# Performance work log

Measured on AMD Instinct MI355X. Metric: run time of the kernel, lower is better.

The kernel has to match this reference:

```python
import jax, jax.numpy as jnp
import numpy as np

H = 56; W = 56; WS = 7; SS = 3; NH = 12; DIM = 384; B = 32
N = WS * WS                      # 49 tokens per window
NW = (H // WS) * (W // WS)       # 64 windows per image
HID = 4 * DIM
EPS = 1e-5


def _rel_index():
    coords = np.stack(np.meshgrid(np.arange(WS), np.arange(WS), indexing='ij'))  # [2,ws,ws]
    cf = coords.reshape(2, -1)
    rel = (cf[:, :, None] - cf[:, None, :]).transpose(1, 2, 0)  # [N,N,2]
    rel[..., 0] += WS - 1
    rel[..., 1] += WS - 1
    rel[..., 0] *= 2 * WS - 1
    return rel.sum(-1).astype(np.int32)  # [N,N] in [0,169)


def _attn_mask():
    img = np.zeros((H, W), np.float32)
    cnt = 0
    sl = (slice(0, -WS), slice(-WS, -SS), slice(-SS, None))
    for h in sl:
        for w in sl:
            img[h, w] = cnt
            cnt += 1
    mw = img.reshape(H // WS, WS, W // WS, WS).transpose(0, 2, 1, 3).reshape(-1, N)  # [nW,N]
    am = mw[:, None, :] - mw[:, :, None]  # [nW,N,N]
    return np.where(am != 0, np.float32(-100.0), np.float32(0.0)).astype(np.float32)


def _ln(x, g, b):
    m = jnp.mean(x, axis=-1, keepdims=True)
    v = jnp.mean(jnp.square(x - m), axis=-1, keepdims=True)
    return (x - m) * jax.lax.rsqrt(v + EPS) * g + b


def setup_inputs() -> dict:
    key = jax.random.key(0)
    ks = jax.random.split(key, 8)
    s = 0.02
    return {
        'x': jax.random.normal(ks[0], (B, H * W, DIM), jnp.float32),
        'qkv_w': jax.random.normal(ks[1], (3 * DIM, DIM), jnp.float32) * s,
        'qkv_b': jnp.zeros((3 * DIM,), jnp.float32),
        'proj_w': jax.random.normal(ks[2], (DIM, DIM), jnp.float32) * s,
        'proj_b': jnp.zeros((DIM,), jnp.float32),
        'rpb_table': jax.random.normal(ks[3], ((2 * WS - 1) ** 2, NH), jnp.float32) * s,
        'ln1_g': jnp.ones((DIM,), jnp.float32),
        'ln1_b': jnp.zeros((DIM,), jnp.float32),
        'fc1_w': jax.random.normal(ks[4], (HID, DIM), jnp.float32) * s,
        'fc1_b': jnp.zeros((HID,), jnp.float32),
        'fc2_w': jax.random.normal(ks[5], (DIM, HID), jnp.float32) * s,
        'fc2_b': jnp.zeros((DIM,), jnp.float32),
        'ln2_g': jnp.ones((DIM,), jnp.float32),
        'ln2_b': jnp.zeros((DIM,), jnp.float32),
        'attn_mask': jnp.asarray(_attn_mask()),
        'rel_idx': jnp.asarray(_rel_index()),
    }


def reference(x, qkv_w, qkv_b, proj_w, proj_b, rpb_table, ln1_g, ln1_b,
              fc1_w, fc1_b, fc2_w, fc2_b, ln2_g, ln2_b, attn_mask, rel_idx):
    Bb, L, C = x.shape
    hd = C // NH
    scale = hd ** -0.5
    shortcut = x
    # cyclic shift
    xs = jnp.roll(x.reshape(Bb, H, W, C), (-SS, -SS), axis=(1, 2))
    # window partition -> [Bb*nW, N, C]
    xw = xs.reshape(Bb, H // WS, WS, W // WS, WS, C).transpose(0, 1, 3, 2, 4, 5).reshape(-1, N, C)
    # qkv
    qkv = (xw @ qkv_w.T + qkv_b).reshape(-1, N, 3, NH, hd).transpose(2, 0, 3, 1, 4)
    q, k, v = qkv[0] * scale, qkv[1], qkv[2]          # [Bb*nW, NH, N, hd]
    attn = jnp.einsum('whnd,whmd->whnm', q, k)        # [Bb*nW, NH, N, N]
    bias = rpb_table[rel_idx.reshape(-1)].reshape(N, N, NH).transpose(2, 0, 1)
    attn = attn + bias[None]
    # shifted-window mask
    attn = attn.reshape(Bb, NW, NH, N, N) + attn_mask[None, :, None]
    attn = jax.nn.softmax(attn.reshape(-1, NH, N, N), axis=-1)
    out = jnp.einsum('whnm,whmd->whnd', attn, v).transpose(0, 2, 1, 3).reshape(-1, N, C)
    out = out @ proj_w.T + proj_b
    # window reverse + roll back
    xs = out.reshape(Bb, H // WS, W // WS, WS, WS, C).transpose(0, 1, 3, 2, 4, 5).reshape(Bb, H, W, C)
    xs = jnp.roll(xs, (SS, SS), axis=(1, 2)).reshape(Bb, L, C)
    # post-norm residuals (as in source: shortcut + norm(attn_out); x += norm(ffn(x)))
    x1 = shortcut + _ln(xs, ln1_g, ln1_b)
    y = jax.nn.gelu(x1 @ fc1_w.T + fc1_b, approximate=False) @ fc2_w.T + fc2_b
    return x1 + _ln(y, ln2_g, ln2_b)
```

## Files before the change

kernel.cpp:

```cpp
#include <hip/hip_runtime.h>
#include <hip/hip_bf16.h>
#include <math.h>

typedef __hip_bfloat16 bf16;
typedef __bf16 bf16x8 __attribute__((ext_vector_type(8)));
typedef float f32x4 __attribute__((ext_vector_type(4)));

#define HH 56
#define WW 56
#define WSZ 7
#define SSH 3
#define NHEAD 12
#define CDIM 384
#define BBATCH 32
#define NTOK 49
#define NWIN 64
#define HIDD 1536
#define HD 32
#define NWTOT (BBATCH*NWIN)
#define MROWS (NWTOT*NTOK)
#define MHALF (MROWS/2)
#define LTOT (HH*WW)
#define EPSLN 1e-5f
#define QSCALE 0.17677669529663687f
#define NEGBIG -1e30f

enum { M_QK = 0, M_V = 1, M_FC1 = 2 };

__device__ __forceinline__ void gload16(const void* g, void* l) {
    __builtin_amdgcn_global_load_lds(
        (const __attribute__((address_space(1))) void*)g,
        (__attribute__((address_space(3))) void*)l, 16, 0, 0);
}

__device__ __forceinline__ unsigned short bfbits(float v) {
    bf16 b = __float2bfloat16(v);
    return *reinterpret_cast<unsigned short*>(&b);
}

__device__ __forceinline__ float fast_gelu(float v) {
    return v / (1.0f + __expf(-1.59576912f * v * fmaf(0.044715f, v * v, 1.0f)));
}

__device__ __forceinline__ int xcd_swz(int orig, int nwg) {
    const int q = nwg >> 3, r = nwg & 7;
    const int xcd = orig & 7, loc = orig >> 3;
    return (xcd < r ? xcd * (q + 1) : r * (q + 1) + (xcd - r) * q) + loc;
}

__global__ __launch_bounds__(256) void cvt_k(const float* __restrict__ src,
                                             bf16* __restrict__ dst, int n) {
    int i = blockIdx.x * 256 + threadIdx.x;
    if (i < n) dst[i] = __float2bfloat16(src[i]);
}

__global__ __launch_bounds__(256)
void tbl_k(const float* __restrict__ rpb, const int* __restrict__ relidx,
           const float* __restrict__ amask, float* __restrict__ tbl) {
    int idx = blockIdx.x * 256 + threadIdx.x;
    int m = idx & 63, n = (idx >> 6) & 63;
    int h = (idx >> 12) % NHEAD, wi = idx / (64 * 64 * NHEAD);
    float v;
    if (m >= NTOK) v = NEGBIG;
    else if (n >= NTOK) v = 0.f;
    else v = rpb[relidx[n * NTOK + m] * NHEAD + h] + amask[((long)wi * NTOK + n) * NTOK + m];
    tbl[idx] = v;
}

__global__ __launch_bounds__(256) void gather_k(const float* __restrict__ x,
                                                bf16* __restrict__ xw, int rbase) {
    int idx = blockIdx.x * 256 + threadIdx.x;
    int rr_l = idx / 96, c4 = (idx % 96) * 4;
    int rr = rbase + rr_l;
    int w = rr / 49, ti = rr % 49;
    int b = w >> 6, wi = w & 63;
    int hy = (wi >> 3) * 7 + ti / 7;
    int hx = (wi & 7) * 7 + ti % 7;
    int sh = hy + SSH; if (sh >= HH) sh -= HH;
    int sw = hx + SSH; if (sw >= WW) sw -= WW;
    float4 v = *(const float4*)&x[((long)b * LTOT + sh * WW + sw) * CDIM + c4];
    ushort4 u = { bfbits(v.x), bfbits(v.y), bfbits(v.z), bfbits(v.w) };
    *(ushort4*)&xw[(long)rr_l * CDIM + c4] = u;
}

template<int MODE, int KDIM, int NTN>
__global__ __launch_bounds__(256, 4)
void mgemm_k(const bf16* __restrict__ A, const bf16* __restrict__ Wt,
             const float* __restrict__ bias, void* __restrict__ Outp)
{
    constexpr bool SWAP = (MODE != M_V);
    __shared__ bf16 As[2][128 * 32];
    __shared__ bf16 Bs[2][128 * 32];
    const int tid = threadIdx.x;
    const int wid = tid >> 6, lane = tid & 63;

    const int gid = xcd_swz(blockIdx.x, gridDim.x);
    const int m0 = (gid / NTN) * 128;
    const int n0 = (gid % NTN) * 128;

    const int strow = lane >> 2, stseg = lane & 3;
    const int swseg = stseg ^ ((strow >> 1) & 3);
    const bf16* Ag = A + (long)(m0 + wid * 32 + strow) * KDIM + swseg * 8;
    const bf16* Wg = Wt + (long)(n0 + wid * 32 + strow) * KDIM + swseg * 8;

    const int wr = (wid >> 1) * 64, wc = (wid & 1) * 64;
    const int l15 = lane & 15, g4 = lane >> 4;
    const int sa = g4 ^ ((l15 >> 1) & 3);

    f32x4 acc[4][4] = {};

    auto STAGE = [&](int b, int t) {
#pragma unroll
        for (int i = 0; i < 2; ++i)
            gload16(Ag + (long)(i * 16) * KDIM + t * 32, &As[b][(wid * 32 + i * 16) * 32]);
#pragma unroll
        for (int i = 0; i < 2; ++i)
            gload16(Wg + (long)(i * 16) * KDIM + t * 32, &Bs[b][(wid * 32 + i * 16) * 32]);
    };

    const int nt = KDIM / 32;
    STAGE(0, 0);
    STAGE(1, 1);
    asm volatile("s_waitcnt vmcnt(4)" ::: "memory");
    __builtin_amdgcn_s_barrier();

    int buf = 0;
    for (int t = 0; t < nt; ++t) {
        bf16x8 af[4], bfr[4];
#pragma unroll
        for (int i = 0; i < 4; ++i) {
            af[i]  = *(const bf16x8*)&As[buf][(wr + i * 16 + l15) * 32 + sa * 8];
            bfr[i] = *(const bf16x8*)&Bs[buf][(wc + i * 16 + l15) * 32 + sa * 8];
        }
        __builtin_amdgcn_sched_barrier(0);
        asm volatile("s_waitcnt lgkmcnt(0)" ::: "memory");
        __builtin_amdgcn_sched_barrier(0);
        __builtin_amdgcn_s_barrier();
        if (t + 2 < nt) STAGE(buf, t + 2);
#pragma unroll
        for (int mi = 0; mi < 4; ++mi)
#pragma unroll
            for (int ni = 0; ni < 4; ++ni) {
                if (SWAP)
                    acc[ni][mi] = __builtin_amdgcn_mfma_f32_16x16x32_bf16(
                        bfr[ni], af[mi], acc[ni][mi], 0, 0, 0);
                else
                    acc[mi][ni] = __builtin_amdgcn_mfma_f32_16x16x32_bf16(
                        af[mi], bfr[ni], acc[mi][ni], 0, 0, 0);
            }
        if (t + 2 < nt) { asm volatile("s_waitcnt vmcnt(4)" ::: "memory"); }
        else            { asm volatile("s_waitcnt vmcnt(0)" ::: "memory"); }
        __builtin_amdgcn_s_barrier();
        buf ^= 1;
    }

    if (MODE == M_V) {
#pragma unroll
        for (int mi = 0; mi < 4; ++mi) {
            const int mb = m0 + wr + mi * 16 + g4 * 4;
            const int wv_ = mb / 49, ti0 = mb - wv_ * 49;
#pragma unroll
            for (int ni = 0; ni < 4; ++ni) {
                const int n = n0 + wc + ni * 16 + l15;
                const int h = n >> 5, d = n & 31;
                const float bn = bias[n];
                float v4[4];
#pragma unroll
                for (int j = 0; j < 4; ++j) v4[j] = acc[mi][ni][j] + bn;
                if (ti0 <= 45) {
                    ushort4 u = { bfbits(v4[0]), bfbits(v4[1]), bfbits(v4[2]), bfbits(v4[3]) };
                    *(ushort4*)&((bf16*)Outp)[(((long)wv_ * NHEAD + h) * HD + d) * 64 + ti0] = u;
                } else {
#pragma unroll
                    for (int j = 0; j < 4; ++j) {
                        const int m = mb + j;
                        const int w2 = m / 49, ti = m - w2 * 49;
                        ((bf16*)Outp)[(((long)w2 * NHEAD + h) * HD + d) * 64 + ti]
                            = __float2bfloat16(v4[j]);
                    }
                }
            }
        }
    } else {
        long rowbase[4];
        int wq_[4], ti_[4];
#pragma unroll
        for (int mi = 0; mi < 4; ++mi) {
            const int m = m0 + wr + mi * 16 + l15;
            if (MODE == M_QK) { wq_[mi] = m / 49; ti_[mi] = m - wq_[mi] * 49; }
            else              { rowbase[mi] = (long)m * HIDD; }
        }
#pragma unroll
        for (int ni = 0; ni < 4; ++ni) {
            const int nb = n0 + wc + ni * 16 + g4 * 4;
            const float4 bn = *(const float4*)&bias[nb];
            const float bb[4] = { bn.x, bn.y, bn.z, bn.w };
#pragma unroll
            for (int mi = 0; mi < 4; ++mi) {
                float v4[4];
#pragma unroll
                for (int j = 0; j < 4; ++j) v4[j] = acc[ni][mi][j] + bb[j];
                if (MODE == M_FC1) {
#pragma unroll
                    for (int j = 0; j < 4; ++j) v4[j] = fast_gelu(v4[j]);
                } else if (MODE == M_QK) {
                    if (nb < CDIM) {
#pragma unroll
                        for (int j = 0; j < 4; ++j) v4[j] *= QSCALE;
                    }
                }
                ushort4 u = { bfbits(v4[0]), bfbits(v4[1]), bfbits(v4[2]), bfbits(v4[3]) };
                if (MODE == M_QK) {
                    const int which = nb >= CDIM;
                    const int hb = (nb - which * CDIM) >> 5, d0 = nb & 31;
                    *(ushort4*)&((bf16*)Outp)[
                        ((((long)wq_[mi] * 2 + which) * NHEAD + hb) * NTOK + ti_[mi]) * HD + d0] = u;
                } else {
                    *(ushort4*)&((bf16*)Outp)[rowbase[mi] + nb] = u;
                }
            }
        }
    }
}

template<int KDIM, bool SCATTER>
__global__ __launch_bounds__(512, 2)
void gemm_ln_k(const bf16* __restrict__ A, const bf16* __restrict__ Wt,
               const float* __restrict__ bias, const bf16* __restrict__ resid,
               const float* __restrict__ lng, const float* __restrict__ lnb,
               float* __restrict__ outf, bf16* __restrict__ outb, int mbase)
{
    __shared__ bf16 As[2][128 * 32];
    __shared__ bf16 Bs[2][384 * 32];
    __shared__ float lnp[1024];
    const int tid = threadIdx.x;
    const int wid = tid >> 6, lane = tid & 63;

    const int m0 = xcd_swz(blockIdx.x, gridDim.x) * 128;

    const int strow = tid >> 2, stseg = tid & 3;
    const int sws = stseg ^ ((strow >> 1) & 3);
    const bf16* Ag = A + (long)(m0 + strow) * KDIM + sws * 8;
    const bf16* Wg = Wt + (long)strow * KDIM + sws * 8;

    const int wm = wid >> 2, wn = wid & 3;
    const int wr = wm * 64, wc = wn * 96;
    const int l15 = lane & 15, g4 = lane >> 4;
    const int sa = g4 ^ ((l15 >> 1) & 3);

    f32x4 acc[6][4] = {};

    auto STAGE = [&](int b, int t) {
        gload16(Ag + t * 32, &As[b][strow * 32 + stseg * 8]);
#pragma unroll
        for (int p = 0; p < 3; ++p)
            gload16(Wg + (long)(p * 128) * KDIM + t * 32,
                    &Bs[b][(p * 128 + strow) * 32 + stseg * 8]);
    };

    const int nt = KDIM / 32;
    STAGE(0, 0);
    STAGE(1, 1);
    asm volatile("s_waitcnt vmcnt(4)" ::: "memory");
    __builtin_amdgcn_s_barrier();

    int buf = 0;
    for (int t = 0; t < nt; ++t) {
        bf16x8 af[4], bfr[6];
#pragma unroll
        for (int i = 0; i < 4; ++i)
            af[i] = *(const bf16x8*)&As[buf][(wr + i * 16 + l15) * 32 + sa * 8];
#pragma unroll
        for (int i = 0; i < 6; ++i)
            bfr[i] = *(const bf16x8*)&Bs[buf][(wc + i * 16 + l15) * 32 + sa * 8];
        __builtin_amdgcn_sched_barrier(0);
        asm volatile("s_waitcnt lgkmcnt(0)" ::: "memory");
        __builtin_amdgcn_sched_barrier(0);
        __builtin_amdgcn_s_barrier();
        if (t + 2 < nt) STAGE(buf, t + 2);
#pragma unroll
        for (int ni = 0; ni < 6; ++ni)
#pragma unroll
            for (int mi = 0; mi < 4; ++mi)
                acc[ni][mi] = __builtin_amdgcn_mfma_f32_16x16x32_bf16(
                    bfr[ni], af[mi], acc[ni][mi], 0, 0, 0);
        if (t + 2 < nt) { asm volatile("s_waitcnt vmcnt(4)" ::: "memory"); }
        else            { asm volatile("s_waitcnt vmcnt(0)" ::: "memory"); }
        __builtin_amdgcn_s_barrier();
        buf ^= 1;
    }

    float psum[4] = {}, psq[4] = {};
#pragma unroll
    for (int ni = 0; ni < 6; ++ni) {
        const int nb = wc + ni * 16 + g4 * 4;
        const float4 bn = *(const float4*)&bias[nb];
        const float bb[4] = { bn.x, bn.y, bn.z, bn.w };
#pragma unroll
        for (int mi = 0; mi < 4; ++mi)
#pragma unroll
            for (int j = 0; j < 4; ++j) {
                float v = acc[ni][mi][j] + bb[j];
                acc[ni][mi][j] = v;
                psum[mi] += v; psq[mi] += v * v;
            }
    }
#pragma unroll
    for (int mi = 0; mi < 4; ++mi) {
        psum[mi] += __shfl_xor(psum[mi], 16); psum[mi] += __shfl_xor(psum[mi], 32);
        psq[mi]  += __shfl_xor(psq[mi], 16);  psq[mi]  += __shfl_xor(psq[mi], 32);
    }
    if (g4 == 0) {
#pragma unroll
        for (int mi = 0; mi < 4; ++mi) {
            const int r = wr + mi * 16 + l15;
            lnp[wn * 128 + r] = psum[mi];
            lnp[512 + wn * 128 + r] = psq[mi];
        }
    }
    __syncthreads();

#pragma unroll
    for (int mi = 0; mi < 4; ++mi) {
        const int r = wr + mi * 16 + l15;
        const float s  = lnp[r] + lnp[128 + r] + lnp[256 + r] + lnp[384 + r];
        const float sq = lnp[512 + r] + lnp[640 + r] + lnp[768 + r] + lnp[896 + r];
        const float mean = s * (1.f / 384.f);
        const float rstd = rsqrtf(sq * (1.f / 384.f) - mean * mean + EPSLN);

        const long rl = m0 + r;
        long dst;
        if (SCATTER) {
            const int m = mbase + (int)rl;
            int w = m / 49, ti = m - w * 49;
            int b = w >> 6, wi = w & 63;
            int hy = (wi >> 3) * 7 + ti / 7;
            int hx = (wi & 7) * 7 + ti % 7;
            int dh = hy + SSH; if (dh >= HH) dh -= HH;
            int dw = hx + SSH; if (dw >= WW) dw -= WW;
            dst = (long)b * LTOT + dh * WW + dw - mbase;
        } else {
            dst = mbase + rl;
        }
#pragma unroll
        for (int ni = 0; ni < 6; ++ni) {
            const int c = wc + ni * 16 + g4 * 4;
            const float4 gv = *(const float4*)&lng[c];
            const float4 bv = *(const float4*)&lnb[c];
            ushort4 xv = *(const ushort4*)&resid[rl * CDIM + c];
            float x0 = __bfloat162float(*(bf16*)&xv.x);
            float x1 = __bfloat162float(*(bf16*)&xv.y);
            float x2 = __bfloat162float(*(bf16*)&xv.z);
            float x3 = __bfloat162float(*(bf16*)&xv.w);
            float r0 = x0 + (acc[ni][mi][0] - mean) * rstd * gv.x + bv.x;
            float r1 = x1 + (acc[ni][mi][1] - mean) * rstd * gv.y + bv.y;
            float r2 = x2 + (acc[ni][mi][2] - mean) * rstd * gv.z + bv.z;
            float r3 = x3 + (acc[ni][mi][3] - mean) * rstd * gv.w + bv.w;
            if (SCATTER) {
                ushort4 u = { bfbits(r0), bfbits(r1), bfbits(r2), bfbits(r3) };
                *(ushort4*)&outb[dst * CDIM + c] = u;
            } else {
                float4 o = { r0, r1, r2, r3 };
                *(float4*)&outf[dst * CDIM + c] = o;
            }
        }
    }
}

__global__ __launch_bounds__(256)
void mattn_k(const bf16* __restrict__ qk, const bf16* __restrict__ vT,
             const float* __restrict__ tbl, bf16* __restrict__ attn_out)
{
    __shared__ bf16 Plds[4][64 * 72];
    const int tid = threadIdx.x, wid = tid >> 6, lane = tid & 63;
    const int t = blockIdx.x * 4 + wid;
    const int w = t / NHEAD, h = t % NHEAD, wi = w & 63;
    const int l15 = lane & 15, g = lane >> 4;
    const bf16* qb = qk + ((long)(w * 2 + 0) * NHEAD + h) * (NTOK * HD);
    const bf16* kb = qk + ((long)(w * 2 + 1) * NHEAD + h) * (NTOK * HD);
    const bf16* vt = vT + ((long)w * NHEAD + h) * (HD * 64);
    const float* Tb = tbl + (long)(wi * NHEAD + h) * 64 * 64;
    char* Pw = (char*)&Plds[wid][0];

    bf16x8 kf[4], qf[4];
#pragma unroll
    for (int i = 0; i < 4; ++i) {
        kf[i] = *(const bf16x8*)&kb[(16 * i + l15) * HD + 8 * g];
        qf[i] = *(const bf16x8*)&qb[(16 * i + l15) * HD + 8 * g];
    }
    f32x4 s[4][4] = {};
#pragma unroll
    for (int mi = 0; mi < 4; ++mi)
#pragma unroll
        for (int ni = 0; ni < 4; ++ni)
            s[mi][ni] = __builtin_amdgcn_mfma_f32_16x16x32_bf16(
                kf[mi], qf[ni], s[mi][ni], 0, 0, 0);

#pragma unroll
    for (int ni = 0; ni < 4; ++ni) {
        const int n = 16 * ni + l15;
#pragma unroll
        for (int mi = 0; mi < 4; ++mi) {
            float4 tv = *(const float4*)&Tb[(long)n * 64 + 16 * mi + 4 * g];
            s[mi][ni][0] += tv.x; s[mi][ni][1] += tv.y;
            s[mi][ni][2] += tv.z; s[mi][ni][3] += tv.w;
        }
        float mx = NEGBIG;
#pragma unroll
        for (int mi = 0; mi < 4; ++mi)
#pragma unroll
            for (int j = 0; j < 4; ++j) mx = fmaxf(mx, s[mi][ni][j]);
        mx = fmaxf(mx, __shfl_xor(mx, 16));
        mx = fmaxf(mx, __shfl_xor(mx, 32));
        float sum = 0.f;
#pragma unroll
        for (int mi = 0; mi < 4; ++mi)
#pragma unroll
            for (int j = 0; j < 4; ++j) {
                float e = expf(s[mi][ni][j] - mx);
                s[mi][ni][j] = e; sum += e;
            }
        sum += __shfl_xor(sum, 16);
        sum += __shfl_xor(sum, 32);
        const float r = 1.0f / sum;
#pragma unroll
        for (int mi = 0; mi < 4; ++mi) {
            ushort4 u;
            u.x = bfbits(s[mi][ni][0] * r);
            u.y = bfbits(s[mi][ni][1] * r);
            u.z = bfbits(s[mi][ni][2] * r);
            u.w = bfbits(s[mi][ni][3] * r);
            *(ushort4*)(Pw + (long)n * 144 + (16 * mi + 4 * g) * 2) = u;
        }
    }

    f32x4 o[4][2] = {};
#pragma unroll
    for (int kk = 0; kk < 2; ++kk) {
        bf16x8 vf[2];
        vf[0] = *(const bf16x8*)&vt[(long)(l15) * 64 + 32 * kk + 8 * g];
        vf[1] = *(const bf16x8*)&vt[(long)(16 + l15) * 64 + 32 * kk + 8 * g];
#pragma unroll
        for (int rt = 0; rt < 4; ++rt) {
            bf16x8 pf = *(const bf16x8*)(Pw + (long)(16 * rt + l15) * 144 + (32 * kk + 8 * g) * 2);
            o[rt][0] = __builtin_amdgcn_mfma_f32_16x16x32_bf16(pf, vf[0], o[rt][0], 0, 0, 0);
            o[rt][1] = __builtin_amdgcn_mfma_f32_16x16x32_bf16(pf, vf[1], o[rt][1], 0, 0, 0);
        }
    }

#pragma unroll
    for (int rt = 0; rt < 4; ++rt)
#pragma unroll
        for (int dt = 0; dt < 2; ++dt)
#pragma unroll
            for (int j = 0; j < 4; ++j) {
                int n = 16 * rt + 4 * g + j;
                if (n < NTOK)
                    attn_out[((long)w * NTOK + n) * CDIM + h * HD + 16 * dt + l15]
                        = __float2bfloat16(o[rt][dt][j]);
            }
}

extern "C" void kernel_launch(void* const* d_in, const int* in_sizes, int n_in,
                              void* d_out, int out_size, void* d_ws, size_t ws_size,
                              hipStream_t stream)
{
    const float* x      = (const float*)d_in[0];
    const float* qkv_w  = (const float*)d_in[1];
    const float* qkv_b  = (const float*)d_in[2];
    const float* proj_w = (const float*)d_in[3];
    const float* proj_b = (const float*)d_in[4];
    const float* rpb    = (const float*)d_in[5];
    const float* ln1_g  = (const float*)d_in[6];
    const float* ln1_b  = (const float*)d_in[7];
    const float* fc1_w  = (const float*)d_in[8];
    const float* fc1_b  = (const float*)d_in[9];
    const float* fc2_w  = (const float*)d_in[10];
    const float* fc2_b  = (const float*)d_in[11];
    const float* ln2_g  = (const float*)d_in[12];
    const float* ln2_b  = (const float*)d_in[13];
    const float* amask  = (const float*)d_in[14];
    const int*   relidx = (const int*)d_in[15];
    float* out = (float*)d_out;
    char*  ws  = (char*)d_ws;

    bf16*  wq    = (bf16*) (ws + 0L);
    bf16*  wp    = (bf16*) (ws + 884736L);
    bf16*  w1    = (bf16*) (ws + 1179648L);
    bf16*  w2    = (bf16*) (ws + 2359296L);
    float* tbl   = (float*)(ws + 3538944L);
    bf16*  xw_h  = (bf16*) (ws + 16121856L);
    bf16*  qkb_h = (bf16*) (ws + 54657024L);
    bf16*  vT_h  = (bf16*) (ws + 131727360L);
    bf16*  att_h = (bf16*) (ws + 182059008L);
    bf16*  x1b_h = (bf16*) (ws + 220594176L);
    bf16*  H1_h  = (bf16*) (ws + 16121856L);

    dim3 b256(256), b512(512);

    cvt_k<<<dim3((3*CDIM*CDIM + 255)/256), b256, 0, stream>>>(qkv_w, wq, 3*CDIM*CDIM);
    cvt_k<<<dim3((CDIM*CDIM + 255)/256), b256, 0, stream>>>(proj_w, wp, CDIM*CDIM);
    cvt_k<<<dim3((HIDD*CDIM + 255)/256), b256, 0, stream>>>(fc1_w, w1, HIDD*CDIM);
    cvt_k<<<dim3((CDIM*HIDD + 255)/256), b256, 0, stream>>>(fc2_w, w2, CDIM*HIDD);
    tbl_k<<<dim3(64*12*64*64/256), b256, 0, stream>>>(rpb, relidx, amask, tbl);

    for (int c = 0; c < 2; ++c) {
        const int mb = c * MHALF;
        gather_k<<<dim3(MHALF * 96 / 256), b256, 0, stream>>>(x, xw_h, mb);
        mgemm_k<M_QK, CDIM, 6><<<dim3((MHALF/128)*6), b256, 0, stream>>>(
            xw_h, wq, qkv_b, (void*)qkb_h);
        mgemm_k<M_V, CDIM, 3><<<dim3((MHALF/128)*3), b256, 0, stream>>>(
            xw_h, wq + (long)2*CDIM*CDIM, qkv_b + 2*CDIM, (void*)vT_h);
        mattn_k<<<dim3(1024 * NHEAD / 4), b256, 0, stream>>>(qkb_h, vT_h, tbl, att_h);
        gemm_ln_k<CDIM, true><<<dim3(MHALF/128), b512, 0, stream>>>(
            att_h, wp, proj_b, xw_h, ln1_g, ln1_b, nullptr, x1b_h, mb);
        mgemm_k<M_FC1, CDIM, 12><<<dim3((MHALF/128)*12), b256, 0, stream>>>(
            x1b_h, w1, fc1_b, (void*)H1_h);
        gemm_ln_k<HIDD, false><<<dim3(MHALF/128), b512, 0, stream>>>(
            H1_h, w2, fc2_b, x1b_h, ln2_g, ln2_b, out, nullptr, mb);
    }
}
```

Baseline: 890.5 us.

## Merge QKV GEMMs, batch attention stage over full M, fuse weight conversions

```diff
diff --git a/kernel.cpp b/kernel.cpp
--- a/kernel.cpp
+++ b/kernel.cpp
@@ -25,8 +25,6 @@
 #define QSCALE 0.17677669529663687f
 #define NEGBIG -1e30f
 
-enum { M_QK = 0, M_V = 1, M_FC1 = 2 };
-
 __device__ __forceinline__ void gload16(const void* g, void* l) {
     __builtin_amdgcn_global_load_lds(
         (const __attribute__((address_space(1))) void*)g,
@@ -48,10 +46,16 @@
     return (xcd < r ? xcd * (q + 1) : r * (q + 1) + (xcd - r) * q) + loc;
 }
 
-__global__ __launch_bounds__(256) void cvt_k(const float* __restrict__ src,
-                                             bf16* __restrict__ dst, int n) {
+__global__ __launch_bounds__(256)
+void cvt4_k(const float* __restrict__ s0, const float* __restrict__ s1,
+            const float* __restrict__ s2, const float* __restrict__ s3,
+            bf16* __restrict__ d0, bf16* __restrict__ d1,
+            bf16* __restrict__ d2, bf16* __restrict__ d3) {
     int i = blockIdx.x * 256 + threadIdx.x;
-    if (i < n) dst[i] = __float2bfloat16(src[i]);
+    if (i < 442368)        d0[i] = __float2bfloat16(s0[i]);
+    else if (i < 589824)  { int j = i - 442368;  d1[j] = __float2bfloat16(s1[j]); }
+    else if (i < 1179648) { int j = i - 589824;  d2[j] = __float2bfloat16(s2[j]); }
+    else                  { int j = i - 1179648; d3[j] = __float2bfloat16(s3[j]); }
 }
 
 __global__ __launch_bounds__(256)
@@ -68,10 +72,9 @@
 }
 
 __global__ __launch_bounds__(256) void gather_k(const float* __restrict__ x,
-                                                bf16* __restrict__ xw, int rbase) {
+                                                bf16* __restrict__ xw) {
     int idx = blockIdx.x * 256 + threadIdx.x;
-    int rr_l = idx / 96, c4 = (idx % 96) * 4;
-    int rr = rbase + rr_l;
+    int rr = idx / 96, c4 = (idx % 96) * 4;
     int w = rr / 49, ti = rr % 49;
     int b = w >> 6, wi = w & 63;
     int hy = (wi >> 3) * 7 + ti / 7;
@@ -80,15 +83,15 @@
     int sw = hx + SSH; if (sw >= WW) sw -= WW;
     float4 v = *(const float4*)&x[((long)b * LTOT + sh * WW + sw) * CDIM + c4];
     ushort4 u = { bfbits(v.x), bfbits(v.y), bfbits(v.z), bfbits(v.w) };
-    *(ushort4*)&xw[(long)rr_l * CDIM + c4] = u;
-}
-
-template<int MODE, int KDIM, int NTN>
+    *(ushort4*)&xw[(long)rr * CDIM + c4] = u;
+}
+
+template<int KDIM, int NTN>
 __global__ __launch_bounds__(256, 4)
-void mgemm_k(const bf16* __restrict__ A, const bf16* __restrict__ Wt,
-             const float* __restrict__ bias, void* __restrict__ Outp)
+void qkv_k(const bf16* __restrict__ A, const bf16* __restrict__ Wt,
+           const float* __restrict__ bias, bf16* __restrict__ qk_out,
+           bf16* __restrict__ vT_out)
 {
-    constexpr bool SWAP = (MODE != M_V);
     __shared__ bf16 As[2][128 * 32];
     __shared__ bf16 Bs[2][128 * 32];
     const int tid = threadIdx.x;
@@ -97,6 +100,7 @@
     const int gid = xcd_swz(blockIdx.x, gridDim.x);
     const int m0 = (gid / NTN) * 128;
     const int n0 = (gid % NTN) * 128;
+    const bool isV = (n0 >= 2 * CDIM);
 
     const int strow = lane >> 2, stseg = lane & 3;
     const int swseg = stseg ^ ((strow >> 1) & 3);
@@ -137,24 +141,28 @@
         __builtin_amdgcn_sched_barrier(0);
         __builtin_amdgcn_s_barrier();
         if (t + 2 < nt) STAGE(buf, t + 2);
-#pragma unroll
-        for (int mi = 0; mi < 4; ++mi)
-#pragma unroll
-            for (int ni = 0; ni < 4; ++ni) {
-                if (SWAP)
+        if (isV) {
+#pragma unroll
+            for (int mi = 0; mi < 4; ++mi)
+#pragma unroll
+                for (int ni = 0; ni < 4; ++ni)
+                    acc[mi][ni] = __builtin_amdgcn_mfma_f32_16x16x32_bf16(
+                        af[mi], bfr[ni], acc[mi][ni], 0, 0, 0);
+        } else {
+#pragma unroll
+            for (int mi = 0; mi < 4; ++mi)
+#pragma unroll
+                for (int ni = 0; ni < 4; ++ni)
                     acc[ni][mi] = __builtin_amdgcn_mfma_f32_16x16x32_bf16(
                         bfr[ni], af[mi], acc[ni][mi], 0, 0, 0);
-                else
-                    acc[mi][ni] = __builtin_amdgcn_mfma_f32_16x16x32_bf16(
-                        af[mi], bfr[ni], acc[mi][ni], 0, 0, 0);
-            }
+        }
         if (t + 2 < nt) { asm volatile("s_waitcnt vmcnt(4)" ::: "memory"); }
         else            { asm volatile("s_waitcnt vmcnt(0)" ::: "memory"); }
         __builtin_amdgcn_s_barrier();
         buf ^= 1;
     }
 
-    if (MODE == M_V) {
+    if (isV) {
 #pragma unroll
         for (int mi = 0; mi < 4; ++mi) {
             const int mb = m0 + wr + mi * 16 + g4 * 4;
@@ -162,63 +170,138 @@
 #pragma unroll
             for (int ni = 0; ni < 4; ++ni) {
                 const int n = n0 + wc + ni * 16 + l15;
-                const int h = n >> 5, d = n & 31;
+                const int nv = n - 2 * CDIM;
+                const int h = nv >> 5, d = nv & 31;
                 const float bn = bias[n];
                 float v4[4];
 #pragma unroll
                 for (int j = 0; j < 4; ++j) v4[j] = acc[mi][ni][j] + bn;
                 if (ti0 <= 45) {
                     ushort4 u = { bfbits(v4[0]), bfbits(v4[1]), bfbits(v4[2]), bfbits(v4[3]) };
-                    *(ushort4*)&((bf16*)Outp)[(((long)wv_ * NHEAD + h) * HD + d) * 64 + ti0] = u;
+                    *(ushort4*)&vT_out[(((long)wv_ * NHEAD + h) * HD + d) * 64 + ti0] = u;
                 } else {
 #pragma unroll
                     for (int j = 0; j < 4; ++j) {
                         const int m = mb + j;
                         const int w2 = m / 49, ti = m - w2 * 49;
-                        ((bf16*)Outp)[(((long)w2 * NHEAD + h) * HD + d) * 64 + ti]
+                        vT_out[(((long)w2 * NHEAD + h) * HD + d) * 64 + ti]
                             = __float2bfloat16(v4[j]);
                     }
                 }
             }
         }
     } else {
-        long rowbase[4];
         int wq_[4], ti_[4];
 #pragma unroll
         for (int mi = 0; mi < 4; ++mi) {
             const int m = m0 + wr + mi * 16 + l15;
-            if (MODE == M_QK) { wq_[mi] = m / 49; ti_[mi] = m - wq_[mi] * 49; }
-            else              { rowbase[mi] = (long)m * HIDD; }
+            wq_[mi] = m / 49; ti_[mi] = m - wq_[mi] * 49;
         }
 #pragma unroll
         for (int ni = 0; ni < 4; ++ni) {
             const int nb = n0 + wc + ni * 16 + g4 * 4;
             const float4 bn = *(const float4*)&bias[nb];
             const float bb[4] = { bn.x, bn.y, bn.z, bn.w };
+            const int which = nb >= CDIM;
+            const int hb = (nb - which * CDIM) >> 5, d0 = nb & 31;
 #pragma unroll
             for (int mi = 0; mi < 4; ++mi) {
                 float v4[4];
 #pragma unroll
                 for (int j = 0; j < 4; ++j) v4[j] = acc[ni][mi][j] + bb[j];
-                if (MODE == M_FC1) {
-#pragma unroll
-                    for (int j = 0; j < 4; ++j) v4[j] = fast_gelu(v4[j]);
-                } else if (MODE == M_QK) {
-                    if (nb < CDIM) {
-#pragma unroll
-                        for (int j = 0; j < 4; ++j) v4[j] *= QSCALE;
-                    }
+                if (!which) {
+#pragma unroll
+                    for (int j = 0; j < 4; ++j) v4[j] *= QSCALE;
                 }
                 ushort4 u = { bfbits(v4[0]), bfbits(v4[1]), bfbits(v4[2]), bfbits(v4[3]) };
-                if (MODE == M_QK) {
-                    const int which = nb >= CDIM;
-                    const int hb = (nb - which * CDIM) >> 5, d0 = nb & 31;
-                    *(ushort4*)&((bf16*)Outp)[
-                        ((((long)wq_[mi] * 2 + which) * NHEAD + hb) * NTOK + ti_[mi]) * HD + d0] = u;
-                } else {
-                    *(ushort4*)&((bf16*)Outp)[rowbase[mi] + nb] = u;
-                }
+                *(ushort4*)&qk_out[
+                    ((((long)wq_[mi] * 2 + which) * NHEAD + hb) * NTOK + ti_[mi]) * HD + d0] = u;
             }
+        }
+    }
+}
+
+template<int KDIM, int NTN>
+__global__ __launch_bounds__(256, 4)
+void fc1_k(const bf16* __restrict__ A, const bf16* __restrict__ Wt,
+           const float* __restrict__ bias, bf16* __restrict__ Outp)
+{
+    __shared__ bf16 As[2][128 * 32];
+    __shared__ bf16 Bs[2][128 * 32];
+    const int tid = threadIdx.x;
+    const int wid = tid >> 6, lane = tid & 63;
+
+    const int gid = xcd_swz(blockIdx.x, gridDim.x);
+    const int m0 = (gid / NTN) * 128;
+    const int n0 = (gid % NTN) * 128;
+
+    const int strow = lane >> 2, stseg = lane & 3;
+    const int swseg = stseg ^ ((strow >> 1) & 3);
+    const bf16* Ag = A + (long)(m0 + wid * 32 + strow) * KDIM + swseg * 8;
+    const bf16* Wg = Wt + (long)(n0 + wid * 32 + strow) * KDIM + swseg * 8;
+
+    const int wr = (wid >> 1) * 64, wc = (wid & 1) * 64;
+    const int l15 = lane & 15, g4 = lane >> 4;
+    const int sa = g4 ^ ((l15 >> 1) & 3);
+
+    f32x4 acc[4][4] = {};
+
+    auto STAGE = [&](int b, int t) {
+#pragma unroll
+        for (int i = 0; i < 2; ++i)
+            gload16(Ag + (long)(i * 16) * KDIM + t * 32, &As[b][(wid * 32 + i * 16) * 32]);
+#pragma unroll
+        for (int i = 0; i < 2; ++i)
+            gload16(Wg + (long)(i * 16) * KDIM + t * 32, &Bs[b][(wid * 32 + i * 16) * 32]);
+    };
+
+    const int nt = KDIM / 32;
+    STAGE(0, 0);
+    STAGE(1, 1);
+    asm volatile("s_waitcnt vmcnt(4)" ::: "memory");
+    __builtin_amdgcn_s_barrier();
+
+    int buf = 0;
+    for (int t = 0; t < nt; ++t) {
+        bf16x8 af[4], bfr[4];
+#pragma unroll
+        for (int i = 0; i < 4; ++i) {
+            af[i]  = *(const bf16x8*)&As[buf][(wr + i * 16 + l15) * 32 + sa * 8];
+            bfr[i] = *(const bf16x8*)&Bs[buf][(wc + i * 16 + l15) * 32 + sa * 8];
+        }
+        __builtin_amdgcn_sched_barrier(0);
+        asm volatile("s_waitcnt lgkmcnt(0)" ::: "memory");
+        __builtin_amdgcn_sched_barrier(0);
+        __builtin_amdgcn_s_barrier();
+        if (t + 2 < nt) STAGE(buf, t + 2);
+#pragma unroll
+        for (int mi = 0; mi < 4; ++mi)
+#pragma unroll
+            for (int ni = 0; ni < 4; ++ni)
+                acc[ni][mi] = __builtin_amdgcn_mfma_f32_16x16x32_bf16(
+                    bfr[ni], af[mi], acc[ni][mi], 0, 0, 0);
+        if (t + 2 < nt) { asm volatile("s_waitcnt vmcnt(4)" ::: "memory"); }
+        else            { asm volatile("s_waitcnt vmcnt(0)" ::: "memory"); }
+        __builtin_amdgcn_s_barrier();
+        buf ^= 1;
+    }
+
+    long rowbase[4];
+#pragma unroll
+    for (int mi = 0; mi < 4; ++mi)
+        rowbase[mi] = (long)(m0 + wr + mi * 16 + l15) * HIDD;
+#pragma unroll
+    for (int ni = 0; ni < 4; ++ni) {
+        const int nb = n0 + wc + ni * 16 + g4 * 4;
+        const float4 bn = *(const float4*)&bias[nb];
+        const float bb[4] = { bn.x, bn.y, bn.z, bn.w };
+#pragma unroll
+        for (int mi = 0; mi < 4; ++mi) {
+            float v4[4];
+#pragma unroll
+            for (int j = 0; j < 4; ++j) v4[j] = fast_gelu(acc[ni][mi][j] + bb[j]);
+            ushort4 u = { bfbits(v4[0]), bfbits(v4[1]), bfbits(v4[2]), bfbits(v4[3]) };
+            *(ushort4*)&Outp[rowbase[mi] + nb] = u;
         }
     }
 }
@@ -226,7 +309,8 @@
 template<int KDIM, bool SCATTER>
 __global__ __launch_bounds__(512, 2)
 void gemm_ln_k(const bf16* __restrict__ A, const bf16* __restrict__ Wt,
-               const float* __restrict__ bias, const bf16* __restrict__ resid,
+               const float* __restrict__ bias, const bf16* __restrict__ residb,
+               const float* __restrict__ residf,
                const float* __restrict__ lng, const float* __restrict__ lnb,
                float* __restrict__ outf, bf16* __restrict__ outb, int mbase)
 {
@@ -331,14 +415,14 @@
         const long rl = m0 + r;
         long dst;
         if (SCATTER) {
-            const int m = mbase + (int)rl;
+            const int m = (int)rl;
             int w = m / 49, ti = m - w * 49;
             int b = w >> 6, wi = w & 63;
             int hy = (wi >> 3) * 7 + ti / 7;
             int hx = (wi & 7) * 7 + ti % 7;
             int dh = hy + SSH; if (dh >= HH) dh -= HH;
             int dw = hx + SSH; if (dw >= WW) dw -= WW;
-            dst = (long)b * LTOT + dh * WW + dw - mbase;
+            dst = (long)b * LTOT + dh * WW + dw;
         } else {
             dst = mbase + rl;
         }
@@ -347,11 +431,17 @@
             const int c = wc + ni * 16 + g4 * 4;
             const float4 gv = *(const float4*)&lng[c];
             const float4 bv = *(const float4*)&lnb[c];
-            ushort4 xv = *(const ushort4*)&resid[rl * CDIM + c];
-            float x0 = __bfloat162float(*(bf16*)&xv.x);
-            float x1 = __bfloat162float(*(bf16*)&xv.y);
-            float x2 = __bfloat162float(*(bf16*)&xv.z);
-            float x3 = __bfloat162float(*(bf16*)&xv.w);
+            float x0, x1, x2, x3;
+            if (SCATTER) {
+                const float4 xv = *(const float4*)&residf[dst * CDIM + c];
+                x0 = xv.x; x1 = xv.y; x2 = xv.z; x3 = xv.w;
+            } else {
+                ushort4 xv = *(const ushort4*)&residb[rl * CDIM + c];
+                x0 = __bfloat162float(*(bf16*)&xv.x);
+                x1 = __bfloat162float(*(bf16*)&xv.y);
+                x2 = __bfloat162float(*(bf16*)&xv.z);
+                x3 = __bfloat162float(*(bf16*)&xv.w);
+            }
             float r0 = x0 + (acc[ni][mi][0] - mean) * rstd * gv.x + bv.x;
             float r1 = x1 + (acc[ni][mi][1] - mean) * rstd * gv.y + bv.y;
             float r2 = x2 + (acc[ni][mi][2] - mean) * rstd * gv.z + bv.z;
@@ -484,39 +574,39 @@
     float* out = (float*)d_out;
     char*  ws  = (char*)d_ws;
 
-    bf16*  wq    = (bf16*) (ws + 0L);
-    bf16*  wp    = (bf16*) (ws + 884736L);
-    bf16*  w1    = (bf16*) (ws + 1179648L);
-    bf16*  w2    = (bf16*) (ws + 2359296L);
-    float* tbl   = (float*)(ws + 3538944L);
-    bf16*  xw_h  = (bf16*) (ws + 16121856L);
-    bf16*  qkb_h = (bf16*) (ws + 54657024L);
-    bf16*  vT_h  = (bf16*) (ws + 131727360L);
-    bf16*  att_h = (bf16*) (ws + 182059008L);
-    bf16*  x1b_h = (bf16*) (ws + 220594176L);
-    bf16*  H1_h  = (bf16*) (ws + 16121856L);
+    bf16*  wq   = (bf16*) (ws + 0L);
+    bf16*  wp   = (bf16*) (ws + 884736L);
+    bf16*  w1   = (bf16*) (ws + 1179648L);
+    bf16*  w2   = (bf16*) (ws + 2359296L);
+    float* tbl  = (float*)(ws + 3538944L);
+    bf16*  xw   = (bf16*) (ws + 16121856L);
+    bf16*  qkb  = (bf16*) (ws + 93192192L);
+    bf16*  vTb  = (bf16*) (ws + 247332864L);
+    bf16*  att  = (bf16*) (ws + 16121856L);
+    bf16*  x1b  = (bf16*) (ws + 93192192L);
+    bf16*  H1   = (bf16*) (ws + 170262528L);
 
     dim3 b256(256), b512(512);
 
-    cvt_k<<<dim3((3*CDIM*CDIM + 255)/256), b256, 0, stream>>>(qkv_w, wq, 3*CDIM*CDIM);
-    cvt_k<<<dim3((CDIM*CDIM + 255)/256), b256, 0, stream>>>(proj_w, wp, CDIM*CDIM);
-    cvt_k<<<dim3((HIDD*CDIM + 255)/256), b256, 0, stream>>>(fc1_w, w1, HIDD*CDIM);
-    cvt_k<<<dim3((CDIM*HIDD + 255)/256), b256, 0, stream>>>(fc2_w, w2, CDIM*HIDD);
+    cvt4_k<<<dim3(1769472 / 256), b256, 0, stream>>>(
+        qkv_w, proj_w, fc1_w, fc2_w, wq, wp, w1, w2);
     tbl_k<<<dim3(64*12*64*64/256), b256, 0, stream>>>(rpb, relidx, amask, tbl);
+    gather_k<<<dim3(MROWS * 96 / 256), b256, 0, stream>>>(x, xw);
+
+    qkv_k<CDIM, 9><<<dim3((MROWS/128)*9), b256, 0, stream>>>(
+        xw, wq, qkv_b, qkb, vTb);
+
+    mattn_k<<<dim3(NWTOT * NHEAD / 4), b256, 0, stream>>>(qkb, vTb, tbl, att);
+
+    gemm_ln_k<CDIM, true><<<dim3(MROWS/128), b512, 0, stream>>>(
+        att, wp, proj_b, nullptr, x, ln1_g, ln1_b, nullptr, x1b, 0);
 
     for (int c = 0; c < 2; ++c) {
         const int mb = c * MHALF;
-        gather_k<<<dim3(MHALF * 96 / 256), b256, 0, stream>>>(x, xw_h, mb);
-        mgemm_k<M_QK, CDIM, 6><<<dim3((MHALF/128)*6), b256, 0, stream>>>(
-            xw_h, wq, qkv_b, (void*)qkb_h);
-        mgemm_k<M_V, CDIM, 3><<<dim3((MHALF/128)*3), b256, 0, stream>>>(
-            xw_h, wq + (long)2*CDIM*CDIM, qkv_b + 2*CDIM, (void*)vT_h);
-        mattn_k<<<dim3(1024 * NHEAD / 4), b256, 0, stream>>>(qkb_h, vT_h, tbl, att_h);
-        gemm_ln_k<CDIM, true><<<dim3(MHALF/128), b512, 0, stream>>>(
-            att_h, wp, proj_b, xw_h, ln1_g, ln1_b, nullptr, x1b_h, mb);
-        mgemm_k<M_FC1, CDIM, 12><<<dim3((MHALF/128)*12), b256, 0, stream>>>(
-            x1b_h, w1, fc1_b, (void*)H1_h);
+        const long off = (long)mb * CDIM;
+        fc1_k<CDIM, 12><<<dim3((MHALF/128)*12), b256, 0, stream>>>(
+            x1b + off, w1, fc1_b, H1);
         gemm_ln_k<HIDD, false><<<dim3(MHALF/128), b512, 0, stream>>>(
-            H1_h, w2, fc2_b, x1b_h, ln2_g, ln2_b, out, nullptr, mb);
-    }
-}
+            H1, w2, fc2_b, x1b + off, nullptr, ln2_g, ln2_b, out, nullptr, mb);
+    }
+}
```

Measured after the change: 1.498 ms. 68.2% more time.
